# Optimization experiments

Hardware: AMD Instinct MI355X
Metric: run time of the kernel (lower is better)

## Reference

```python
import jax, jax.numpy as jnp
import numpy as np

N = 300000
IN_C = 64
OUT_C = 128
N_Z = 8
B, H, W = 4, 256, 256


def setup_inputs() -> dict:
    key = jax.random.key(0)
    k = jax.random.split(key, 7)
    std = 1.0 / np.sqrt(IN_C)
    return {
        "features": jax.random.normal(k[0], (N, IN_C), dtype=jnp.float32),
        "kernel": jax.random.uniform(k[1], (N_Z, IN_C, OUT_C), dtype=jnp.float32, minval=-std, maxval=std),
        "bias": jnp.zeros((1, OUT_C), dtype=jnp.float32),
        "batch_idx": jax.random.randint(k[2], (N,), 0, B, dtype=jnp.int32),
        "d0_idx": jax.random.randint(k[3], (N,), 0, H, dtype=jnp.int32),
        "d1_idx": jax.random.randint(k[4], (N,), 0, W, dtype=jnp.int32),
        "z_idx": jax.random.randint(k[5], (N,), 0, N_Z, dtype=jnp.int32),
    }


def reference(features, kernel, bias, batch_idx, d0_idx, d1_idx, z_idx):
    # stride s = 1 on the drcv path, so //s is identity
    z = jnp.clip(z_idx, 0, N_Z - 1)
    flat_bev = batch_idx * (H * W) + d0_idx * W + d1_idx  # [N]
    # per-point learned matmul: features[n] @ kernel[z[n]]
    # (computed as a small fixed loop over n_z height bins to avoid
    #  materializing the [N, in_c, out_c] gathered kernel)
    bev_feat = jnp.zeros((features.shape[0], OUT_C), dtype=features.dtype)
    for zz in range(N_Z):
        bev_feat = bev_feat + jnp.where((z == zz)[:, None], features @ kernel[zz], 0.0)
    bev_feat = bev_feat + bias
    # scatter_add into dense BEV
    bev = jnp.zeros((B * H * W, OUT_C), dtype=features.dtype).at[flat_bev].add(bev_feat)
    return bev.reshape(B, H, W, OUT_C).transpose(0, 3, 1, 2)
```

## Files before the change

### kernel.cpp

```cpp
#include <hip/hip_runtime.h>

#define PPB   128
#define NZ    8
#define INC   64
#define OUTC  128
#define NB    4
#define HH    256
#define WWD   256
#define HWD   (HH * WWD)
#define NSEG  (NB * HH)
#define NCELL (NB * HH * WWD)

typedef __attribute__((ext_vector_type(8))) short bf16x8;
typedef __attribute__((ext_vector_type(4))) float f32x4;

__device__ __forceinline__ unsigned bf16_rne(float x) {
    unsigned u = __float_as_uint(x);
    return (u + 0x7FFFu + ((u >> 16) & 1u)) >> 16;
}
__device__ __forceinline__ unsigned pack2(float lo, float hi) {
    return bf16_rne(lo) | (bf16_rne(hi) << 16);
}

__global__ __launch_bounds__(256) void wprep_kernel(const float* __restrict__ kw,
                                                    unsigned short* __restrict__ wt,
                                                    int* __restrict__ meta,
                                                    int* __restrict__ cellhist) {
    int z = blockIdx.x;
    int t = threadIdx.x;
    if (z == 0 && t < 32) meta[t] = 0;
    {
        int4 zero4 = make_int4(0, 0, 0, 0);
        int4* ch4 = (int4*)cellhist;
        int idx0 = (z * 256 + t) * 32;
#pragma unroll
        for (int i = 0; i < 32; ++i) ch4[idx0 + i] = zero4;
    }
    const float* src = kw + (size_t)z * INC * OUTC;
    unsigned short* dst = wt + (size_t)z * OUTC * INC;
    for (int c = t; c < OUTC; c += 256) {
#pragma unroll
        for (int k = 0; k < INC; k += 2) {
            float a = src[(size_t)k * OUTC + c];
            float b = src[(size_t)(k + 1) * OUTC + c];
            *(unsigned*)&dst[(size_t)c * INC + k] = pack2(a, b);
        }
    }
}

__global__ void hist_kernel(const int* __restrict__ z_idx, const int* __restrict__ batch_idx,
                            const int* __restrict__ d0_idx, const int* __restrict__ d1_idx,
                            int* __restrict__ counts, int* __restrict__ cellhist, int n) {
    __shared__ int lc[NZ];
    int t = threadIdx.x;
    if (t < NZ) lc[t] = 0;
    __syncthreads();
    int i = blockIdx.x * blockDim.x + t;
    if (i < n) {
        int z = z_idx[i]; z = z < 0 ? 0 : (z > NZ - 1 ? NZ - 1 : z);
        atomicAdd(&lc[z], 1);
        int cell = (batch_idx[i] * HH + d0_idx[i]) * WWD + d1_idx[i];
        atomicAdd(&cellhist[cell], 1);
    }
    __syncthreads();
    if (t < NZ && lc[t] > 0) atomicAdd(&counts[t], lc[t]);
}

__global__ __launch_bounds__(256) void scan_local(const int* __restrict__ cellhist,
                                                  int* __restrict__ cellstart,
                                                  int* __restrict__ chunksum,
                                                  const int* __restrict__ counts,
                                                  int* __restrict__ pstart) {
    if (blockIdx.x == 0 && threadIdx.x == 0) {
        int off = 0;
        for (int z = 0; z < NZ; ++z) {
            pstart[z] = off;
            off += ((counts[z] + PPB - 1) / PPB) * PPB;
        }
        pstart[NZ] = off;
    }
    __shared__ int ts[256];
    int t = threadIdx.x;
    int base = blockIdx.x * 1024 + t * 4;
    int4 v = *(const int4*)&cellhist[base];
    int s = v.x + v.y + v.z + v.w;
    ts[t] = s;
    __syncthreads();
    for (int d = 1; d < 256; d <<= 1) {
        int x = (t >= d) ? ts[t - d] : 0;
        __syncthreads();
        ts[t] += x;
        __syncthreads();
    }
    int excl = ts[t] - s;
    int4 o;
    o.x = excl; o.y = excl + v.x; o.z = o.y + v.y; o.w = o.z + v.z;
    *(int4*)&cellstart[base] = o;
    if (t == 255) chunksum[blockIdx.x] = ts[255];
}

__global__ __launch_bounds__(256) void scan_add2(int* __restrict__ cellstart,
                                                 const int* __restrict__ chunksum) {
    __shared__ int ts[256];
    int t = threadIdx.x;
    int b = blockIdx.x;
    ts[t] = (t < b) ? chunksum[t] : 0;
    __syncthreads();
    for (int d = 128; d > 0; d >>= 1) {
        if (t < d) ts[t] += ts[t + d];
        __syncthreads();
    }
    int off = ts[0];
    if (off == 0) return;
    int base = b * 1024 + t * 4;
    int4 v = *(int4*)&cellstart[base];
    v.x += off; v.y += off; v.z += off; v.w += off;
    *(int4*)&cellstart[base] = v;
}

__global__ void scatter_kernel(const int* __restrict__ z_idx, const int* __restrict__ batch_idx,
                               const int* __restrict__ d0_idx, const int* __restrict__ d1_idx,
                               const int* __restrict__ pstart, int* __restrict__ cursors,
                               int* __restrict__ cellstart,
                               int* __restrict__ bins, int* __restrict__ segpos, int n) {
    __shared__ int lc[NZ];
    __shared__ int lbase[NZ];
    int t = threadIdx.x;
    if (t < NZ) lc[t] = 0;
    __syncthreads();
    int i = blockIdx.x * blockDim.x + t;
    int z = 0, rank = 0;
    bool valid = (i < n);
    if (valid) {
        z = z_idx[i]; z = z < 0 ? 0 : (z > NZ - 1 ? NZ - 1 : z);
        rank = atomicAdd(&lc[z], 1);
    }
    __syncthreads();
    if (t < NZ) lbase[t] = (lc[t] > 0) ? atomicAdd(&cursors[t], lc[t]) : 0;
    __syncthreads();
    if (valid) {
        int slot = pstart[z] + lbase[z] + rank;
        bins[slot] = i;
        int cell = (batch_idx[i] * HH + d0_idx[i]) * WWD + d1_idx[i];
        int r2 = atomicAdd(&cellstart[cell], 1);
        segpos[slot] = 1 + r2;
    }
}

__global__ __launch_bounds__(256) void gemm_kernel(
        const float* __restrict__ features, const unsigned short* __restrict__ wt,
        const float* __restrict__ bias, const int* __restrict__ counts,
        const int* __restrict__ pstart, const int* __restrict__ bins,
        const int* __restrict__ segpos, unsigned* __restrict__ bevf) {
    __shared__ __align__(16) char lbuf[32768];
    __shared__ int psl[PPB];
    char* Abf = lbuf;
    char* Wbf = lbuf + 16384;

    int start = blockIdx.x * PPB;
    int total = pstart[NZ];
    if (start >= total) return;
    int z = 0;
#pragma unroll
    for (int zz = 1; zz < NZ; ++zz)
        if (start >= pstart[zz]) z = zz;
    int limit = pstart[z] + counts[z] - start;
    if (limit <= 0) return;

    int tid = threadIdx.x;
    if (tid < PPB) psl[tid] = (tid < limit) ? segpos[start + tid] : 0;

    {
        int r = tid >> 1, half = tid & 1;
        int raw = (r < limit) ? bins[start + r] : 0;
        int nid = raw < 0 ? 0 : raw;
        const float4* fp = (const float4*)(features + (size_t)nid * INC) + half * 8;
        float4 f[8];
#pragma unroll
        for (int q = 0; q < 8; ++q) f[q] = fp[q];
        unsigned u[16];
#pragma unroll
        for (int m = 0; m < 8; ++m) {
            u[2 * m]     = pack2(f[m].x, f[m].y);
            u[2 * m + 1] = pack2(f[m].z, f[m].w);
        }
#pragma unroll
        for (int ch = 0; ch < 4; ++ch) {
            int off = (r * 128 + half * 64 + ch * 16) ^ ((r & 7) << 4);
            uint4 val = make_uint4(u[4 * ch], u[4 * ch + 1], u[4 * ch + 2], u[4 * ch + 3]);
            *(uint4*)(Abf + off) = val;
        }
    }
    {
        const uint4* src = (const uint4*)(wt + (size_t)z * OUTC * INC);
#pragma unroll
        for (int i = 0; i < 4; ++i) {
            int s = tid + 256 * i;
            int c = s >> 3, ch = s & 7;
            int off = (c * 128 + ch * 16) ^ ((c & 7) << 4);
            *(uint4*)(Wbf + off) = src[s];
        }
    }
    __syncthreads();

    int wv_ = tid >> 6, l = tid & 63;
    int wr = wv_ >> 1, wc = wv_ & 1;

    f32x4 acc[4][4];
#pragma unroll
    for (int i = 0; i < 4; ++i)
#pragma unroll
        for (int j = 0; j < 4; ++j) acc[i][j] = (f32x4){0.f, 0.f, 0.f, 0.f};

#pragma unroll
    for (int kc = 0; kc < 2; ++kc) {
        bf16x8 af[4], bfr[4];
#pragma unroll
        for (int pb = 0; pb < 4; ++pb) {
            int p = wr * 64 + pb * 16 + (l & 15);
            int off = (p * 128 + kc * 64 + (l >> 4) * 16) ^ ((p & 7) << 4);
            af[pb] = *(const bf16x8*)(Abf + off);
        }
#pragma unroll
        for (int cb = 0; cb < 4; ++cb) {
            int c = wc * 64 + cb * 16 + (l & 15);
            int off = (c * 128 + kc * 64 + (l >> 4) * 16) ^ ((c & 7) << 4);
            bfr[cb] = *(const bf16x8*)(Wbf + off);
        }
#pragma unroll
        for (int pb = 0; pb < 4; ++pb)
#pragma unroll
            for (int cb = 0; cb < 4; ++cb)
                acc[pb][cb] = __builtin_amdgcn_mfma_f32_16x16x32_bf16(
                    af[pb], bfr[cb], acc[pb][cb], 0, 0, 0);
    }
    __syncthreads();

    float bias_c[4];
#pragma unroll
    for (int cb = 0; cb < 4; ++cb) bias_c[cb] = bias[wc * 64 + cb * 16 + (l & 15)];

#pragma unroll
    for (int pb = 0; pb < 4; ++pb) {
#pragma unroll
        for (int cb = 0; cb < 4; ++cb) {
            int c = wc * 64 + cb * 16 + (l & 15);
#pragma unroll
            for (int q = 0; q < 4; ++q) {
                int prow = wr * 64 + pb * 16 + (l >> 4) * 4 + q;
                float v = acc[pb][cb][q] + bias_c[cb];
                int byteoff = (prow * 256 + c * 2) ^ (((prow >> 2) & 3) << 5);
                *(unsigned short*)(lbuf + byteoff) = (unsigned short)bf16_rne(v);
            }
        }
    }
    __syncthreads();

#pragma unroll
    for (int j = 0; j < 8; ++j) {
        int s = j * 256 + tid;
        int prow = s >> 4, chunk = s & 15;
        int byteoff = (prow * 256 + chunk * 16) ^ (((prow >> 2) & 3) << 5);
        uint4 val = *(const uint4*)(lbuf + byteoff);
        int pos = psl[prow];
        *((uint4*)(bevf + (size_t)pos * 64) + chunk) = val;
    }
}

__global__ __launch_bounds__(512) void reduce_kernel(
        const unsigned* __restrict__ bevf, const int* __restrict__ cellstart,
        float* __restrict__ out) {
    __shared__ unsigned tile[256 * 64];
    int t = threadIdx.x;
    int blk = blockIdx.x;
    blk = (blk & 7) * (NSEG / 8) + (blk >> 3);
    int seg = blk;

    int qw = t >> 4;
    int m  = t & 15;
    int w0 = qw * 8;
    int cell0 = seg * WWD + w0;

    int idx = cell0 + m - 1;
    int bound = 0;
    if (m <= 8) bound = (idx < 0) ? 0 : cellstart[idx];
    int r0 = __shfl(bound, 0, 16);
    int r1 = __shfl(bound, 8, 16);

    float f[8];
#pragma unroll
    for (int i = 0; i < 8; ++i) f[i] = 0.f;
    int j = 0;
    int ce = __shfl(bound, 1, 16);

    for (int r = r0; r < r1; r += 4) {
        uint4 v[4];
#pragma unroll
        for (int u = 0; u < 4; ++u) {
            int rr = (r + u < r1) ? r + u : r1 - 1;
            v[u] = *(const uint4*)&bevf[(size_t)(rr + 1) * 64 + 4 * m];
        }
#pragma unroll
        for (int u = 0; u < 4; ++u) {
            if (r + u >= r1) break;
            while (r + u >= ce) {
                int w = w0 + j;
                int sb = w + (w >> 2);
                tile[w * 64 + ((4 * m + 0 + sb) & 63)] = pack2(f[0], f[1]);
                tile[w * 64 + ((4 * m + 1 + sb) & 63)] = pack2(f[2], f[3]);
                tile[w * 64 + ((4 * m + 2 + sb) & 63)] = pack2(f[4], f[5]);
                tile[w * 64 + ((4 * m + 3 + sb) & 63)] = pack2(f[6], f[7]);
#pragma unroll
                for (int i = 0; i < 8; ++i) f[i] = 0.f;
                ++j;
                ce = __shfl(bound, j + 1, 16);
            }
            f[0] += __uint_as_float(v[u].x << 16);
            f[1] += __uint_as_float(v[u].x & 0xFFFF0000u);
            f[2] += __uint_as_float(v[u].y << 16);
            f[3] += __uint_as_float(v[u].y & 0xFFFF0000u);
            f[4] += __uint_as_float(v[u].z << 16);
            f[5] += __uint_as_float(v[u].z & 0xFFFF0000u);
            f[6] += __uint_as_float(v[u].w << 16);
            f[7] += __uint_as_float(v[u].w & 0xFFFF0000u);
        }
    }
    while (j < 8) {
        int w = w0 + j;
        int sb = w + (w >> 2);
        tile[w * 64 + ((4 * m + 0 + sb) & 63)] = pack2(f[0], f[1]);
        tile[w * 64 + ((4 * m + 1 + sb) & 63)] = pack2(f[2], f[3]);
        tile[w * 64 + ((4 * m + 2 + sb) & 63)] = pack2(f[4], f[5]);
        tile[w * 64 + ((4 * m + 3 + sb) & 63)] = pack2(f[6], f[7]);
#pragma unroll
        for (int i = 0; i < 8; ++i) f[i] = 0.f;
        ++j;
    }
    __syncthreads();

    int wv = t >> 6, l = t & 63;
    int b = seg >> 8, h = seg & 255;
    float* ob = out + (size_t)b * OUTC * HWD + (size_t)h * WWD;
#pragma unroll
    for (int r = 0; r < 16; ++r) {
        int c = wv + 8 * r;
        int d = c >> 1;
        bool hi = c & 1;
        unsigned v0 = tile[(4 * l + 0) * 64 + ((d + 5 * l + 0) & 63)];
        unsigned v1 = tile[(4 * l + 1) * 64 + ((d + 5 * l + 1) & 63)];
        unsigned v2 = tile[(4 * l + 2) * 64 + ((d + 5 * l + 2) & 63)];
        unsigned v3 = tile[(4 * l + 3) * 64 + ((d + 5 * l + 3) & 63)];
        float4 o;
        o.x = __uint_as_float(hi ? (v0 & 0xFFFF0000u) : (v0 << 16));
        o.y = __uint_as_float(hi ? (v1 & 0xFFFF0000u) : (v1 << 16));
        o.z = __uint_as_float(hi ? (v2 & 0xFFFF0000u) : (v2 << 16));
        o.w = __uint_as_float(hi ? (v3 & 0xFFFF0000u) : (v3 << 16));
        *(float4*)(ob + (size_t)c * HWD + 4 * l) = o;
    }
}

__global__ __launch_bounds__(256) void naive_kernel(
        const float* __restrict__ features, const float* __restrict__ kw,
        const float* __restrict__ bias,
        const int* __restrict__ bidx, const int* __restrict__ d0,
        const int* __restrict__ d1, const int* __restrict__ zi,
        float* __restrict__ out, int n) {
    long long gid = (long long)blockIdx.x * blockDim.x + threadIdx.x;
    int pid = (int)(gid >> 7);
    int c   = (int)(gid & (OUTC - 1));
    if (pid >= n) return;
    int z = zi[pid]; z = z < 0 ? 0 : (z > NZ - 1 ? NZ - 1 : z);
    const float4* fp = (const float4*)(features + (size_t)pid * INC);
    const float* wp = kw + (size_t)z * INC * OUTC + c;
    float a0 = bias[c], a1 = 0.f, a2 = 0.f, a3 = 0.f;
#pragma unroll
    for (int i = 0; i < INC / 4; ++i) {
        float4 f = fp[i];
        a0 += f.x * wp[(size_t)(4 * i + 0) * OUTC];
        a1 += f.y * wp[(size_t)(4 * i + 1) * OUTC];
        a2 += f.z * wp[(size_t)(4 * i + 2) * OUTC];
        a3 += f.w * wp[(size_t)(4 * i + 3) * OUTC];
    }
    float acc = (a0 + a1) + (a2 + a3);
    size_t oidx = ((size_t)bidx[pid] * OUTC + c) * HWD + (size_t)d0[pid] * WWD + d1[pid];
    unsafeAtomicAdd(&out[oidx], acc);
}

extern "C" void kernel_launch(void* const* d_in, const int* in_sizes, int n_in,
                              void* d_out, int out_size, void* d_ws, size_t ws_size,
                              hipStream_t stream) {
    const float* features = (const float*)d_in[0];
    const float* kw       = (const float*)d_in[1];
    const float* bias     = (const float*)d_in[2];
    const int* batch_idx  = (const int*)d_in[3];
    const int* d0_idx     = (const int*)d_in[4];
    const int* d1_idx     = (const int*)d_in[5];
    const int* z_idx      = (const int*)d_in[6];
    float* out = (float*)d_out;
    int n = in_sizes[0] / INC;

    size_t binsElems = (size_t)n + (size_t)NZ * PPB;
    size_t bevfBytes = (binsElems + 1) * OUTC * 2;
    size_t wtOff     = (bevfBytes + 255) & ~(size_t)255;
    size_t metaOff   = wtOff + (size_t)NZ * OUTC * INC * 2;
    size_t chOff     = (metaOff + 32 * 4 + 255) & ~(size_t)255;
    size_t csOff     = chOff + (size_t)NCELL * 4;
    size_t ckOff     = csOff + (size_t)(NCELL + 4) * 4;
    size_t binsOff   = (ckOff + 256 * 4 + 255) & ~(size_t)255;
    size_t posOff    = binsOff + binsElems * 4;
    size_t need      = posOff + binsElems * 4 + 16;

    if (ws_size >= need) {
        char* ws = (char*)d_ws;
        unsigned* bevf = (unsigned*)ws;
        unsigned short* wt = (unsigned short*)(ws + wtOff);
        int* meta      = (int*)(ws + metaOff);
        int* counts    = meta;
        int* cursors   = meta + 8;
        int* pstart    = meta + 16;
        int* cellhist  = (int*)(ws + chOff);
        int* cellstart = (int*)(ws + csOff);
        int* chunksum  = (int*)(ws + ckOff);
        int* bins      = (int*)(ws + binsOff);
        int* segpos    = (int*)(ws + posOff);

        int gb = (n + 255) / 256;
        wprep_kernel<<<NZ, 256, 0, stream>>>(kw, wt, meta, cellhist);
        hist_kernel<<<gb, 256, 0, stream>>>(z_idx, batch_idx, d0_idx, d1_idx,
                                            counts, cellhist, n);
        scan_local<<<256, 256, 0, stream>>>(cellhist, cellstart, chunksum,
                                            counts, pstart);
        scan_add2<<<256, 256, 0, stream>>>(cellstart, chunksum);
        scatter_kernel<<<gb, 256, 0, stream>>>(z_idx, batch_idx, d0_idx, d1_idx,
                                               pstart, cursors, cellstart,
                                               bins, segpos, n);

        int nblk = (int)((binsElems + PPB - 1) / PPB) + 1;
        gemm_kernel<<<nblk, 256, 0, stream>>>(features, wt, bias, counts, pstart,
                                              bins, segpos, bevf);

        reduce_kernel<<<NSEG, 512, 0, stream>>>(bevf, cellstart, out);
    } else {
        hipMemsetAsync(out, 0, (size_t)out_size * sizeof(float), stream);
        long long threads = (long long)n * OUTC;
        int gb = (int)((threads + 255) / 256);
        naive_kernel<<<gb, 256, 0, stream>>>(features, kw, bias, batch_idx, d0_idx,
                                             d1_idx, z_idx, out, n);
    }
}
```

Before: 146.7 us.

## Fold chunk-offset scan into scatter and reduce; load GEMM weights directly to registers

```diff
diff --git a/kernel.cpp b/kernel.cpp
--- a/kernel.cpp
+++ b/kernel.cpp
@@ -99,34 +99,31 @@
     if (t == 255) chunksum[blockIdx.x] = ts[255];
 }
 
-__global__ __launch_bounds__(256) void scan_add2(int* __restrict__ cellstart,
-                                                 const int* __restrict__ chunksum) {
-    __shared__ int ts[256];
-    int t = threadIdx.x;
-    int b = blockIdx.x;
-    ts[t] = (t < b) ? chunksum[t] : 0;
-    __syncthreads();
-    for (int d = 128; d > 0; d >>= 1) {
-        if (t < d) ts[t] += ts[t + d];
-        __syncthreads();
-    }
-    int off = ts[0];
-    if (off == 0) return;
-    int base = b * 1024 + t * 4;
-    int4 v = *(int4*)&cellstart[base];
-    v.x += off; v.y += off; v.z += off; v.w += off;
-    *(int4*)&cellstart[base] = v;
-}
-
-__global__ void scatter_kernel(const int* __restrict__ z_idx, const int* __restrict__ batch_idx,
-                               const int* __restrict__ d0_idx, const int* __restrict__ d1_idx,
-                               const int* __restrict__ pstart, int* __restrict__ cursors,
-                               int* __restrict__ cellstart,
-                               int* __restrict__ bins, int* __restrict__ segpos, int n) {
+__global__ __launch_bounds__(256) void scatter_kernel(
+        const int* __restrict__ z_idx, const int* __restrict__ batch_idx,
+        const int* __restrict__ d0_idx, const int* __restrict__ d1_idx,
+        const int* __restrict__ pstart, int* __restrict__ cursors,
+        int* __restrict__ cellstart, const int* __restrict__ chunksum,
+        int* __restrict__ bins, int* __restrict__ segpos, int n) {
     __shared__ int lc[NZ];
     __shared__ int lbase[NZ];
+    __shared__ int cko[256];
     int t = threadIdx.x;
     if (t < NZ) lc[t] = 0;
+    {
+        int s = chunksum[t];
+        cko[t] = s;
+        __syncthreads();
+        for (int d = 1; d < 256; d <<= 1) {
+            int x = (t >= d) ? cko[t - d] : 0;
+            __syncthreads();
+            cko[t] += x;
+            __syncthreads();
+        }
+        int excl = cko[t] - s;
+        __syncthreads();
+        cko[t] = excl;
+    }
     __syncthreads();
     int i = blockIdx.x * blockDim.x + t;
     int z = 0, rank = 0;
@@ -143,7 +140,7 @@
         bins[slot] = i;
         int cell = (batch_idx[i] * HH + d0_idx[i]) * WWD + d1_idx[i];
         int r2 = atomicAdd(&cellstart[cell], 1);
-        segpos[slot] = 1 + r2;
+        segpos[slot] = 1 + r2 + cko[cell >> 10];
     }
 }
 
@@ -155,7 +152,6 @@
     __shared__ __align__(16) char lbuf[32768];
     __shared__ int psl[PPB];
     char* Abf = lbuf;
-    char* Wbf = lbuf + 16384;
 
     int start = blockIdx.x * PPB;
     int total = pstart[NZ];
@@ -168,7 +164,18 @@
     if (limit <= 0) return;
 
     int tid = threadIdx.x;
+    int wv_ = tid >> 6, l = tid & 63;
+    int wr = wv_ >> 1, wc = wv_ & 1;
+
     if (tid < PPB) psl[tid] = (tid < limit) ? segpos[start + tid] : 0;
+
+    bf16x8 bfr[4][2];
+#pragma unroll
+    for (int cb = 0; cb < 4; ++cb)
+#pragma unroll
+        for (int kc = 0; kc < 2; ++kc)
+            bfr[cb][kc] = *(const bf16x8*)&wt[(size_t)z * OUTC * INC +
+                (size_t)(wc * 64 + cb * 16 + (l & 15)) * INC + kc * 32 + (l >> 4) * 8];
 
     {
         int r = tid >> 1, half = tid & 1;
@@ -191,20 +198,7 @@
             *(uint4*)(Abf + off) = val;
         }
     }
-    {
-        const uint4* src = (const uint4*)(wt + (size_t)z * OUTC * INC);
-#pragma unroll
-        for (int i = 0; i < 4; ++i) {
-            int s = tid + 256 * i;
-            int c = s >> 3, ch = s & 7;
-            int off = (c * 128 + ch * 16) ^ ((c & 7) << 4);
-            *(uint4*)(Wbf + off) = src[s];
-        }
-    }
-    __syncthreads();
-
-    int wv_ = tid >> 6, l = tid & 63;
-    int wr = wv_ >> 1, wc = wv_ & 1;
+    __syncthreads();
 
     f32x4 acc[4][4];
 #pragma unroll
@@ -214,7 +208,7 @@
 
 #pragma unroll
     for (int kc = 0; kc < 2; ++kc) {
-        bf16x8 af[4], bfr[4];
+        bf16x8 af[4];
 #pragma unroll
         for (int pb = 0; pb < 4; ++pb) {
             int p = wr * 64 + pb * 16 + (l & 15);
@@ -222,17 +216,11 @@
             af[pb] = *(const bf16x8*)(Abf + off);
         }
 #pragma unroll
-        for (int cb = 0; cb < 4; ++cb) {
-            int c = wc * 64 + cb * 16 + (l & 15);
-            int off = (c * 128 + kc * 64 + (l >> 4) * 16) ^ ((c & 7) << 4);
-            bfr[cb] = *(const bf16x8*)(Wbf + off);
-        }
-#pragma unroll
         for (int pb = 0; pb < 4; ++pb)
 #pragma unroll
             for (int cb = 0; cb < 4; ++cb)
                 acc[pb][cb] = __builtin_amdgcn_mfma_f32_16x16x32_bf16(
-                    af[pb], bfr[cb], acc[pb][cb], 0, 0, 0);
+                    af[pb], bfr[cb][kc], acc[pb][cb], 0, 0, 0);
     }
     __syncthreads();
 
@@ -269,9 +257,26 @@
 
 __global__ __launch_bounds__(512) void reduce_kernel(
         const unsigned* __restrict__ bevf, const int* __restrict__ cellstart,
-        float* __restrict__ out) {
+        const int* __restrict__ chunksum, float* __restrict__ out) {
     __shared__ unsigned tile[256 * 64];
+    __shared__ int cko[512];
     int t = threadIdx.x;
+    {
+        int s = (t < 256) ? chunksum[t] : 0;
+        cko[t] = s;
+        __syncthreads();
+        for (int d = 1; d < 512; d <<= 1) {
+            int x = (t >= d) ? cko[t - d] : 0;
+            __syncthreads();
+            cko[t] += x;
+            __syncthreads();
+        }
+        int excl = cko[t] - s;
+        __syncthreads();
+        cko[t] = excl;
+        __syncthreads();
+    }
+
     int blk = blockIdx.x;
     blk = (blk & 7) * (NSEG / 8) + (blk >> 3);
     int seg = blk;
@@ -283,7 +288,7 @@
 
     int idx = cell0 + m - 1;
     int bound = 0;
-    if (m <= 8) bound = (idx < 0) ? 0 : cellstart[idx];
+    if (m <= 8) bound = (idx < 0) ? 0 : cellstart[idx] + cko[idx >> 10];
     int r0 = __shfl(bound, 0, 16);
     int r1 = __shfl(bound, 8, 16);
 
@@ -430,16 +435,15 @@
                                             counts, cellhist, n);
         scan_local<<<256, 256, 0, stream>>>(cellhist, cellstart, chunksum,
                                             counts, pstart);
-        scan_add2<<<256, 256, 0, stream>>>(cellstart, chunksum);
         scatter_kernel<<<gb, 256, 0, stream>>>(z_idx, batch_idx, d0_idx, d1_idx,
-                                               pstart, cursors, cellstart,
+                                               pstart, cursors, cellstart, chunksum,
                                                bins, segpos, n);
 
         int nblk = (int)((binsElems + PPB - 1) / PPB) + 1;
         gemm_kernel<<<nblk, 256, 0, stream>>>(features, wt, bias, counts, pstart,
                                               bins, segpos, bevf);
 
-        reduce_kernel<<<NSEG, 512, 0, stream>>>(bevf, cellstart, out);
+        reduce_kernel<<<NSEG, 512, 0, stream>>>(bevf, cellstart, chunksum, out);
     } else {
         hipMemsetAsync(out, 0, (size_t)out_size * sizeof(float), stream);
         long long threads = (long long)n * OUTC;
```

After: 144.7 us. About the same (-1.3%).
